# Performance work log

Hardware: AMD Instinct MI355X
Metric: run time of the kernel (lower is better)

## Reference

```python
import jax, jax.numpy as jnp
import numpy as np

SCALE = 0.08838834764831845  # 1/sqrt(128)


def setup_inputs() -> dict:
    key = jax.random.key(0)
    k1, k2, k3, k4 = jax.random.split(key, 4)
    B, Sq, H, D = 1, 2048, 32, 128
    Skv, K = 4096, 256
    return {
        "q": jax.random.normal(k1, (B, Sq, H, D), jnp.float32),
        "kv": jax.random.normal(k2, (B, Skv, 2, D), jnp.float32),  # stacked K,V (MQA)
        "attn_sink": jax.random.normal(k3, (H,), jnp.float32),
        "topk_idxs": jax.random.randint(k4, (B, Sq, K), 0, Skv),
    }


def reference(q, kv, attn_sink, topk_idxs):
    # q:        [B, Sq, H, D]
    # kv:       [B, Skv, 2, D]  (index 0 = keys, 1 = values; shared across heads)
    # topk_idxs:[B, Sq, K]      per-query selected KV positions
    # attn_sink:[H]             per-head sink logit added to the softmax denominator
    B = q.shape[0]
    # Gather selected KV per query: [B, Sq, K, 2, D]
    gathered = kv[jnp.arange(B)[:, None, None], topk_idxs]
    k = gathered[..., 0, :]  # [B, Sq, K, D]
    v = gathered[..., 1, :]  # [B, Sq, K, D]

    scores = jnp.einsum("bqhd,bqkd->bqhk", q, k) * SCALE  # [B, Sq, H, K]
    sink = attn_sink[None, None, :, None]                  # [1, 1, H, 1]

    # Numerically stable softmax over K selected tokens + sink logit.
    m = jnp.maximum(jnp.max(scores, axis=-1, keepdims=True), sink)
    e = jnp.exp(scores - m)
    denom = jnp.sum(e, axis=-1, keepdims=True) + jnp.exp(sink - m)
    probs = e / denom                                      # sink absorbs leftover mass

    out = jnp.einsum("bqhk,bqkd->bqhd", probs, v)          # [B, Sq, H, D]
    return out
```

## Files before the change

kernel.cpp:

```cpp
#include <hip/hip_runtime.h>
#include <hip/hip_bf16.h>

#define SQ 2048
#define NH 32
#define DH 128
#define NK 256
#define SCALE 0.08838834764831845f
#define LOG2E 1.4426950408889634f

typedef __attribute__((ext_vector_type(8))) __bf16 bf16x8;
typedef __attribute__((ext_vector_type(4))) float floatx4;

#define QS_STRIDE 136
#define KS_STRIDE 136
#define VB_STRIDE 72
#define PB_STRIDE 264

#define OFF_KV   16896
#define OFF_TOPK 35328
#define OFF_SINK 36352
#define OFF_RED  36480
#define OFF_RED2 36992
#define SMEM_SZ  37504

__device__ __forceinline__ unsigned pk_bf16(float a, float b) {
  union { __hip_bfloat162 h2; unsigned u; } c;
  c.h2 = __float22bfloat162_rn(make_float2(a, b));
  return c.u;
}

__device__ __forceinline__ float fast_exp2(float x) {
#if __has_builtin(__builtin_amdgcn_exp2f)
  return __builtin_amdgcn_exp2f(x);
#else
  return exp2f(x);
#endif
}

template <int CTRL>
__device__ __forceinline__ float dpp_rot(float x) {
  int i = __builtin_bit_cast(int, x);
  i = __builtin_amdgcn_mov_dpp(i, CTRL, 0xF, 0xF, true);
  return __builtin_bit_cast(float, i);
}
#define RED16_MAX(v) { v = fmaxf(v, dpp_rot<0x121>(v)); v = fmaxf(v, dpp_rot<0x122>(v)); \
                       v = fmaxf(v, dpp_rot<0x124>(v)); v = fmaxf(v, dpp_rot<0x128>(v)); }
#define RED16_SUM(v) { v += dpp_rot<0x121>(v); v += dpp_rot<0x122>(v); \
                       v += dpp_rot<0x124>(v); v += dpp_rot<0x128>(v); }

__global__ __launch_bounds__(256) void kv_to_bf16(const float* __restrict__ kv,
                                                  unsigned short* __restrict__ kvb) {
  int i = blockIdx.x * 256 + threadIdx.x;
  float4 f = ((const float4*)kv)[i];
  uint2 o = { pk_bf16(f.x, f.y), pk_bf16(f.z, f.w) };
  ((uint2*)kvb)[i] = o;
}

struct KR { uint4 v[4]; };
struct VR { uint4 a, b, c, d; };

__device__ __forceinline__ KR k_load(const unsigned short* __restrict__ kvb,
                                     const int* __restrict__ tks, int c, int tid) {
  int r = tid >> 2, seg = tid & 3;
  int idx = tks[c * 64 + r];
  const uint4* p = (const uint4*)(kvb + (size_t)idx * 256 + seg * 32);
  KR k;
#pragma unroll
  for (int i = 0; i < 4; i++) k.v[i] = p[i];
  return k;
}

__device__ __forceinline__ void k_write(unsigned short* kvbuf, const KR& k, int tid) {
  int r = tid >> 2, seg = tid & 3;
  uint4* d = (uint4*)&kvbuf[r * KS_STRIDE + seg * 32];
#pragma unroll
  for (int i = 0; i < 4; i++) d[i] = k.v[i];
}

__device__ __forceinline__ VR v_load(const unsigned short* __restrict__ kvb,
                                     const int* tks, int c, int tid) {
  int rg = tid & 15, dg = tid >> 4;
  int r0 = rg * 4, d0 = dg * 8;
  int4 i4 = *(const int4*)&tks[c * 64 + r0];
  VR v;
  v.a = *(const uint4*)(kvb + (size_t)i4.x * 256 + 128 + d0);
  v.b = *(const uint4*)(kvb + (size_t)i4.y * 256 + 128 + d0);
  v.c = *(const uint4*)(kvb + (size_t)i4.z * 256 + 128 + d0);
  v.d = *(const uint4*)(kvb + (size_t)i4.w * 256 + 128 + d0);
  return v;
}

__device__ __forceinline__ void v_write(unsigned short* kvbuf, const VR& v, int tid) {
  int rg = tid & 15, dg = tid >> 4;
  int r0 = rg * 4, d0 = dg * 8;
  const unsigned* pa = (const unsigned*)&v.a;
  const unsigned* pb = (const unsigned*)&v.b;
  const unsigned* pc = (const unsigned*)&v.c;
  const unsigned* pd = (const unsigned*)&v.d;
#pragma unroll
  for (int w = 0; w < 4; w++) {
    unsigned lo01 = __builtin_amdgcn_perm(pb[w], pa[w], 0x05040100u);
    unsigned lo23 = __builtin_amdgcn_perm(pd[w], pc[w], 0x05040100u);
    unsigned hi01 = __builtin_amdgcn_perm(pb[w], pa[w], 0x07060302u);
    unsigned hi23 = __builtin_amdgcn_perm(pd[w], pc[w], 0x07060302u);
    uint2 lo = { lo01, lo23 }, hi = { hi01, hi23 };
    *(uint2*)&kvbuf[(d0 + 2 * w) * VB_STRIDE + r0] = lo;
    *(uint2*)&kvbuf[(d0 + 2 * w + 1) * VB_STRIDE + r0] = hi;
  }
}

__device__ __forceinline__ void gemm1(const unsigned short* kvbuf,
                                      const bf16x8 af[2][4], int nrow, int quad,
                                      floatx4& a0, floatx4& a1) {
  a0 = (floatx4){0.f, 0.f, 0.f, 0.f};
  a1 = (floatx4){0.f, 0.f, 0.f, 0.f};
#pragma unroll
  for (int ks = 0; ks < 4; ks++) {
    bf16x8 b = *(const bf16x8*)&kvbuf[nrow * KS_STRIDE + ks * 32 + quad * 8];
    a0 = __builtin_amdgcn_mfma_f32_16x16x32_bf16(af[0][ks], b, a0, 0, 0, 0);
    a1 = __builtin_amdgcn_mfma_f32_16x16x32_bf16(af[1][ks], b, a1, 0, 0, 0);
  }
}

__device__ __forceinline__ void pv_chunk(const unsigned short* pbuf,
                                         const unsigned short* kvbuf, int c,
                                         int wave, int quad, int l16,
                                         floatx4 oacc[2][2]) {
#pragma unroll
  for (int ks = 0; ks < 2; ks++) {
    int kof = c * 64 + ks * 32 + quad * 8;
    bf16x8 a0 = *(const bf16x8*)&pbuf[l16 * PB_STRIDE + kof];
    bf16x8 a1 = *(const bf16x8*)&pbuf[(16 + l16) * PB_STRIDE + kof];
    int kl = ks * 32 + quad * 8;
    bf16x8 b0 = *(const bf16x8*)&kvbuf[(wave * 32 + l16) * VB_STRIDE + kl];
    bf16x8 b1 = *(const bf16x8*)&kvbuf[(wave * 32 + 16 + l16) * VB_STRIDE + kl];
    oacc[0][0] = __builtin_amdgcn_mfma_f32_16x16x32_bf16(a0, b0, oacc[0][0], 0, 0, 0);
    oacc[0][1] = __builtin_amdgcn_mfma_f32_16x16x32_bf16(a0, b1, oacc[0][1], 0, 0, 0);
    oacc[1][0] = __builtin_amdgcn_mfma_f32_16x16x32_bf16(a1, b0, oacc[1][0], 0, 0, 0);
    oacc[1][1] = __builtin_amdgcn_mfma_f32_16x16x32_bf16(a1, b1, oacc[1][1], 0, 0, 0);
  }
}

__global__ __launch_bounds__(256, 4) void sparse_attn_kernel(
    const float* __restrict__ q, const unsigned short* __restrict__ kvb,
    const float* __restrict__ sink, const int* __restrict__ topk,
    float* __restrict__ out) {
  __shared__ __align__(16) char smem[SMEM_SZ];
  unsigned short* qs    = (unsigned short*)smem;
  unsigned short* pbuf  = (unsigned short*)smem;
  unsigned short* kvbuf = (unsigned short*)(smem + OFF_KV);
  int*   topk_s = (int*)(smem + OFF_TOPK);
  float* sink_s = (float*)(smem + OFF_SINK);
  float* red    = (float*)(smem + OFF_RED);
  float* red2   = (float*)(smem + OFF_RED2);

  const int tid = threadIdx.x;
  const int s = blockIdx.x;
  const int wave = tid >> 6;
  const int lane = tid & 63;
  const int quad = lane >> 4;
  const int l16 = lane & 15;
  const int* tkg = topk + (size_t)s * NK;

  topk_s[tid] = tkg[tid];
  if (tid < 32) sink_s[tid] = sink[tid] * LOG2E;
  {
    int r = tid >> 2, seg = tid & 3;
    int idx = tkg[r];
    const uint4* p = (const uint4*)(kvb + (size_t)idx * 256 + seg * 32);
    uint4* d = (uint4*)&kvbuf[r * KS_STRIDE + seg * 32];
#pragma unroll
    for (int i = 0; i < 4; i++) d[i] = p[i];
  }
  {
    const float QSC = SCALE * LOG2E;
    const float* qp = q + (size_t)s * (NH * DH);
    int h = tid >> 3, d0 = (tid & 7) * 16;
    const float4* src = (const float4*)(qp + h * DH + d0);
    float4 f0 = src[0], f1 = src[1], f2 = src[2], f3 = src[3];
    uint4 o0 = { pk_bf16(f0.x * QSC, f0.y * QSC), pk_bf16(f0.z * QSC, f0.w * QSC),
                 pk_bf16(f1.x * QSC, f1.y * QSC), pk_bf16(f1.z * QSC, f1.w * QSC) };
    uint4 o1 = { pk_bf16(f2.x * QSC, f2.y * QSC), pk_bf16(f2.z * QSC, f2.w * QSC),
                 pk_bf16(f3.x * QSC, f3.y * QSC), pk_bf16(f3.z * QSC, f3.w * QSC) };
    *(uint4*)&qs[h * QS_STRIDE + d0] = o0;
    *(uint4*)&qs[h * QS_STRIDE + d0 + 8] = o1;
  }
  KR k1 = k_load(kvb, tkg, 1, tid);
  __syncthreads();

  bf16x8 afrag[2][4];
#pragma unroll
  for (int mt = 0; mt < 2; mt++)
#pragma unroll
    for (int ks = 0; ks < 4; ks++)
      afrag[mt][ks] =
          *(const bf16x8*)&qs[(mt * 16 + l16) * QS_STRIDE + ks * 32 + quad * 8];

  const int nrow = wave * 16 + l16;

  floatx4 sc[4][2];
  gemm1(kvbuf, afrag, nrow, quad, sc[0][0], sc[0][1]);
  __syncthreads();
  k_write(kvbuf, k1, tid);
  KR k2 = k_load(kvb, topk_s, 2, tid);
  __syncthreads();

  gemm1(kvbuf, afrag, nrow, quad, sc[1][0], sc[1][1]);
  __syncthreads();
  k_write(kvbuf, k2, tid);
  KR k3 = k_load(kvb, topk_s, 3, tid);
  __syncthreads();

  gemm1(kvbuf, afrag, nrow, quad, sc[2][0], sc[2][1]);
  __syncthreads();
  k_write(kvbuf, k3, tid);
  VR v0 = v_load(kvb, topk_s, 0, tid);
  __syncthreads();

  gemm1(kvbuf, afrag, nrow, quad, sc[3][0], sc[3][1]);
  __syncthreads();
  v_write(kvbuf, v0, tid);
  VR v1 = v_load(kvb, topk_s, 1, tid);

  float mh[2][4];
#pragma unroll
  for (int mt = 0; mt < 2; mt++)
#pragma unroll
    for (int r = 0; r < 4; r++) {
      float v = fmaxf(fmaxf(sc[0][mt][r], sc[1][mt][r]),
                      fmaxf(sc[2][mt][r], sc[3][mt][r]));
      RED16_MAX(v);
      mh[mt][r] = v;
    }
  if (l16 == 0) {
#pragma unroll
    for (int mt = 0; mt < 2; mt++)
#pragma unroll
      for (int r = 0; r < 4; r++)
        red[wave * 32 + mt * 16 + quad * 4 + r] = mh[mt][r];
  }
  __syncthreads();
#pragma unroll
  for (int mt = 0; mt < 2; mt++)
#pragma unroll
    for (int r = 0; r < 4; r++) {
      int h = mt * 16 + quad * 4 + r;
      float v = sink_s[h];
#pragma unroll
      for (int w = 0; w < 4; w++) v = fmaxf(v, red[w * 32 + h]);
      mh[mt][r] = v;
    }
  float ps[2][4];
#pragma unroll
  for (int mt = 0; mt < 2; mt++)
#pragma unroll
    for (int r = 0; r < 4; r++) {
      float acc = 0.f;
#pragma unroll
      for (int c = 0; c < 4; c++) {
        float e = fast_exp2(sc[c][mt][r] - mh[mt][r]);
        sc[c][mt][r] = e;
        acc += e;
      }
      RED16_SUM(acc);
      ps[mt][r] = acc;
    }
  if (l16 == 0) {
#pragma unroll
    for (int mt = 0; mt < 2; mt++)
#pragma unroll
      for (int r = 0; r < 4; r++)
        red2[wave * 32 + mt * 16 + quad * 4 + r] = ps[mt][r];
  }
  __syncthreads();
  float inv[2][4];
#pragma unroll
  for (int mt = 0; mt < 2; mt++)
#pragma unroll
    for (int r = 0; r < 4; r++) {
      int h = mt * 16 + quad * 4 + r;
      float dd = fast_exp2(sink_s[h] - mh[mt][r]);
#pragma unroll
      for (int w = 0; w < 4; w++) dd += red2[w * 32 + h];
      inv[mt][r] = 1.0f / dd;
    }
#pragma unroll
  for (int c = 0; c < 4; c++)
#pragma unroll
    for (int mt = 0; mt < 2; mt++) {
      int col = c * 64 + wave * 16 + l16;
      unsigned short* pb = &pbuf[(mt * 16 + quad * 4) * PB_STRIDE + col];
      unsigned p01 = pk_bf16(sc[c][mt][0], sc[c][mt][1]);
      unsigned p23 = pk_bf16(sc[c][mt][2], sc[c][mt][3]);
      pb[0] = (unsigned short)p01;
      pb[PB_STRIDE] = (unsigned short)(p01 >> 16);
      pb[2 * PB_STRIDE] = (unsigned short)p23;
      pb[3 * PB_STRIDE] = (unsigned short)(p23 >> 16);
    }
  __syncthreads();

  floatx4 oacc[2][2];
#pragma unroll
  for (int mt = 0; mt < 2; mt++)
#pragma unroll
    for (int nt = 0; nt < 2; nt++)
      oacc[mt][nt] = (floatx4){0.f, 0.f, 0.f, 0.f};

  pv_chunk(pbuf, kvbuf, 0, wave, quad, l16, oacc);
  __syncthreads();
  v_write(kvbuf, v1, tid);
  VR v2 = v_load(kvb, topk_s, 2, tid);
  __syncthreads();

  pv_chunk(pbuf, kvbuf, 1, wave, quad, l16, oacc);
  __syncthreads();
  v_write(kvbuf, v2, tid);
  VR v3 = v_load(kvb, topk_s, 3, tid);
  __syncthreads();

  pv_chunk(pbuf, kvbuf, 2, wave, quad, l16, oacc);
  __syncthreads();
  v_write(kvbuf, v3, tid);
  __syncthreads();

  pv_chunk(pbuf, kvbuf, 3, wave, quad, l16, oacc);

  {
    float* op = out + (size_t)s * (NH * DH);
#pragma unroll
    for (int mt = 0; mt < 2; mt++)
#pragma unroll
      for (int nt = 0; nt < 2; nt++)
#pragma unroll
        for (int r4 = 0; r4 < 4; r4++) {
          int h = mt * 16 + quad * 4 + r4;
          int d = wave * 32 + nt * 16 + l16;
          op[h * DH + d] = oacc[mt][nt][r4] * inv[mt][r4];
        }
  }
}

extern "C" void kernel_launch(void* const* d_in, const int* in_sizes, int n_in,
                              void* d_out, int out_size, void* d_ws, size_t ws_size,
                              hipStream_t stream) {
  (void)in_sizes; (void)n_in; (void)out_size; (void)ws_size;
  const float* q    = (const float*)d_in[0];
  const float* kv   = (const float*)d_in[1];
  const float* sink = (const float*)d_in[2];
  const int*   topk = (const int*)d_in[3];
  float* out = (float*)d_out;
  unsigned short* kvb = (unsigned short*)d_ws;

  kv_to_bf16<<<dim3(1024), dim3(256), 0, stream>>>(kv, kvb);
  sparse_attn_kernel<<<dim3(SQ), dim3(256), 0, stream>>>(q, kvb, sink, topk, out);
}
```

Measured before the change: 113.9 us.

## Load K and Q fragments directly from global memory, skipping LDS staging

The QK^T stage now reads each K row's MFMA B-fragment straight from the bf16 KV buffer in global memory, using per-lane top-k indices, instead of staging K chunks through shared memory with barriers. Q is also converted to bf16 directly into registers, and sink values and top-k indices are read from global memory rather than shared copies. This removes many __syncthreads and LDS round trips in the score phase. The cost is uncoalesced 16-byte gathers per lane that rely on L2/L1 hits, plus the V staging now overlaps the score GEMMs. Since vbuf does not alias pbuf, writing V chunk 0 during the score phase appears safe.

```diff
diff --git a/kernel.cpp b/kernel.cpp
--- a/kernel.cpp
+++ b/kernel.cpp
@@ -11,17 +11,13 @@
 typedef __attribute__((ext_vector_type(8))) __bf16 bf16x8;
 typedef __attribute__((ext_vector_type(4))) float floatx4;
 
-#define QS_STRIDE 136
-#define KS_STRIDE 136
 #define VB_STRIDE 72
 #define PB_STRIDE 264
 
-#define OFF_KV   16896
-#define OFF_TOPK 35328
-#define OFF_SINK 36352
-#define OFF_RED  36480
-#define OFF_RED2 36992
-#define SMEM_SZ  37504
+#define OFF_VB   16896
+#define OFF_RED  35328
+#define OFF_RED2 35840
+#define SMEM_SZ  36352
 
 __device__ __forceinline__ unsigned pk_bf16(float a, float b) {
   union { __hip_bfloat162 h2; unsigned u; } c;
@@ -56,32 +52,13 @@
   ((uint2*)kvb)[i] = o;
 }
 
-struct KR { uint4 v[4]; };
 struct VR { uint4 a, b, c, d; };
 
-__device__ __forceinline__ KR k_load(const unsigned short* __restrict__ kvb,
-                                     const int* __restrict__ tks, int c, int tid) {
-  int r = tid >> 2, seg = tid & 3;
-  int idx = tks[c * 64 + r];
-  const uint4* p = (const uint4*)(kvb + (size_t)idx * 256 + seg * 32);
-  KR k;
-#pragma unroll
-  for (int i = 0; i < 4; i++) k.v[i] = p[i];
-  return k;
-}
-
-__device__ __forceinline__ void k_write(unsigned short* kvbuf, const KR& k, int tid) {
-  int r = tid >> 2, seg = tid & 3;
-  uint4* d = (uint4*)&kvbuf[r * KS_STRIDE + seg * 32];
-#pragma unroll
-  for (int i = 0; i < 4; i++) d[i] = k.v[i];
-}
-
 __device__ __forceinline__ VR v_load(const unsigned short* __restrict__ kvb,
-                                     const int* tks, int c, int tid) {
+                                     const int* __restrict__ tkg, int c, int tid) {
   int rg = tid & 15, dg = tid >> 4;
   int r0 = rg * 4, d0 = dg * 8;
-  int4 i4 = *(const int4*)&tks[c * 64 + r0];
+  int4 i4 = *(const int4*)&tkg[c * 64 + r0];
   VR v;
   v.a = *(const uint4*)(kvb + (size_t)i4.x * 256 + 128 + d0);
   v.b = *(const uint4*)(kvb + (size_t)i4.y * 256 + 128 + d0);
@@ -90,7 +67,7 @@
   return v;
 }
 
-__device__ __forceinline__ void v_write(unsigned short* kvbuf, const VR& v, int tid) {
+__device__ __forceinline__ void v_write(unsigned short* vbuf, const VR& v, int tid) {
   int rg = tid & 15, dg = tid >> 4;
   int r0 = rg * 4, d0 = dg * 8;
   const unsigned* pa = (const unsigned*)&v.a;
@@ -104,26 +81,27 @@
     unsigned hi01 = __builtin_amdgcn_perm(pb[w], pa[w], 0x07060302u);
     unsigned hi23 = __builtin_amdgcn_perm(pd[w], pc[w], 0x07060302u);
     uint2 lo = { lo01, lo23 }, hi = { hi01, hi23 };
-    *(uint2*)&kvbuf[(d0 + 2 * w) * VB_STRIDE + r0] = lo;
-    *(uint2*)&kvbuf[(d0 + 2 * w + 1) * VB_STRIDE + r0] = hi;
-  }
-}
-
-__device__ __forceinline__ void gemm1(const unsigned short* kvbuf,
-                                      const bf16x8 af[2][4], int nrow, int quad,
-                                      floatx4& a0, floatx4& a1) {
+    *(uint2*)&vbuf[(d0 + 2 * w) * VB_STRIDE + r0] = lo;
+    *(uint2*)&vbuf[(d0 + 2 * w + 1) * VB_STRIDE + r0] = hi;
+  }
+}
+
+__device__ __forceinline__ void gemm1_direct(const unsigned short* __restrict__ kvb,
+                                             int idx, const bf16x8 af[2][4], int quad,
+                                             floatx4& a0, floatx4& a1) {
+  const unsigned short* kp = kvb + (size_t)idx * 256 + quad * 8;
   a0 = (floatx4){0.f, 0.f, 0.f, 0.f};
   a1 = (floatx4){0.f, 0.f, 0.f, 0.f};
 #pragma unroll
   for (int ks = 0; ks < 4; ks++) {
-    bf16x8 b = *(const bf16x8*)&kvbuf[nrow * KS_STRIDE + ks * 32 + quad * 8];
+    bf16x8 b = *(const bf16x8*)(kp + ks * 32);
     a0 = __builtin_amdgcn_mfma_f32_16x16x32_bf16(af[0][ks], b, a0, 0, 0, 0);
     a1 = __builtin_amdgcn_mfma_f32_16x16x32_bf16(af[1][ks], b, a1, 0, 0, 0);
   }
 }
 
 __device__ __forceinline__ void pv_chunk(const unsigned short* pbuf,
-                                         const unsigned short* kvbuf, int c,
+                                         const unsigned short* vbuf, int c,
                                          int wave, int quad, int l16,
                                          floatx4 oacc[2][2]) {
 #pragma unroll
@@ -132,8 +110,8 @@
     bf16x8 a0 = *(const bf16x8*)&pbuf[l16 * PB_STRIDE + kof];
     bf16x8 a1 = *(const bf16x8*)&pbuf[(16 + l16) * PB_STRIDE + kof];
     int kl = ks * 32 + quad * 8;
-    bf16x8 b0 = *(const bf16x8*)&kvbuf[(wave * 32 + l16) * VB_STRIDE + kl];
-    bf16x8 b1 = *(const bf16x8*)&kvbuf[(wave * 32 + 16 + l16) * VB_STRIDE + kl];
+    bf16x8 b0 = *(const bf16x8*)&vbuf[(wave * 32 + l16) * VB_STRIDE + kl];
+    bf16x8 b1 = *(const bf16x8*)&vbuf[(wave * 32 + 16 + l16) * VB_STRIDE + kl];
     oacc[0][0] = __builtin_amdgcn_mfma_f32_16x16x32_bf16(a0, b0, oacc[0][0], 0, 0, 0);
     oacc[0][1] = __builtin_amdgcn_mfma_f32_16x16x32_bf16(a0, b1, oacc[0][1], 0, 0, 0);
     oacc[1][0] = __builtin_amdgcn_mfma_f32_16x16x32_bf16(a1, b0, oacc[1][0], 0, 0, 0);
@@ -146,13 +124,10 @@
     const float* __restrict__ sink, const int* __restrict__ topk,
     float* __restrict__ out) {
   __shared__ __align__(16) char smem[SMEM_SZ];
-  unsigned short* qs    = (unsigned short*)smem;
-  unsigned short* pbuf  = (unsigned short*)smem;
-  unsigned short* kvbuf = (unsigned short*)(smem + OFF_KV);
-  int*   topk_s = (int*)(smem + OFF_TOPK);
-  float* sink_s = (float*)(smem + OFF_SINK);
-  float* red    = (float*)(smem + OFF_RED);
-  float* red2   = (float*)(smem + OFF_RED2);
+  unsigned short* pbuf = (unsigned short*)smem;
+  unsigned short* vbuf = (unsigned short*)(smem + OFF_VB);
+  float* red  = (float*)(smem + OFF_RED);
+  float* red2 = (float*)(smem + OFF_RED2);
 
   const int tid = threadIdx.x;
   const int s = blockIdx.x;
@@ -162,65 +137,40 @@
   const int l16 = lane & 15;
   const int* tkg = topk + (size_t)s * NK;
 
-  topk_s[tid] = tkg[tid];
-  if (tid < 32) sink_s[tid] = sink[tid] * LOG2E;
-  {
-    int r = tid >> 2, seg = tid & 3;
-    int idx = tkg[r];
-    const uint4* p = (const uint4*)(kvb + (size_t)idx * 256 + seg * 32);
-    uint4* d = (uint4*)&kvbuf[r * KS_STRIDE + seg * 32];
-#pragma unroll
-    for (int i = 0; i < 4; i++) d[i] = p[i];
-  }
-  {
-    const float QSC = SCALE * LOG2E;
-    const float* qp = q + (size_t)s * (NH * DH);
-    int h = tid >> 3, d0 = (tid & 7) * 16;
-    const float4* src = (const float4*)(qp + h * DH + d0);
-    float4 f0 = src[0], f1 = src[1], f2 = src[2], f3 = src[3];
-    uint4 o0 = { pk_bf16(f0.x * QSC, f0.y * QSC), pk_bf16(f0.z * QSC, f0.w * QSC),
-                 pk_bf16(f1.x * QSC, f1.y * QSC), pk_bf16(f1.z * QSC, f1.w * QSC) };
-    uint4 o1 = { pk_bf16(f2.x * QSC, f2.y * QSC), pk_bf16(f2.z * QSC, f2.w * QSC),
-                 pk_bf16(f3.x * QSC, f3.y * QSC), pk_bf16(f3.z * QSC, f3.w * QSC) };
-    *(uint4*)&qs[h * QS_STRIDE + d0] = o0;
-    *(uint4*)&qs[h * QS_STRIDE + d0 + 8] = o1;
-  }
-  KR k1 = k_load(kvb, tkg, 1, tid);
-  __syncthreads();
-
+  float snk[2][4];
+#pragma unroll
+  for (int mt = 0; mt < 2; mt++)
+#pragma unroll
+    for (int r = 0; r < 4; r++)
+      snk[mt][r] = sink[mt * 16 + quad * 4 + r] * LOG2E;
+
+  int kidx[4];
+#pragma unroll
+  for (int c = 0; c < 4; c++) kidx[c] = tkg[c * 64 + wave * 16 + l16];
+
+  const float QSC = SCALE * LOG2E;
+  const float* qp = q + (size_t)s * (NH * DH);
   bf16x8 afrag[2][4];
 #pragma unroll
   for (int mt = 0; mt < 2; mt++)
 #pragma unroll
-    for (int ks = 0; ks < 4; ks++)
-      afrag[mt][ks] =
-          *(const bf16x8*)&qs[(mt * 16 + l16) * QS_STRIDE + ks * 32 + quad * 8];
-
-  const int nrow = wave * 16 + l16;
+    for (int ks = 0; ks < 4; ks++) {
+      const float* base = qp + (mt * 16 + l16) * DH + ks * 32 + quad * 8;
+      float4 f0 = ((const float4*)base)[0];
+      float4 f1 = ((const float4*)base)[1];
+      uint4 u = { pk_bf16(f0.x * QSC, f0.y * QSC), pk_bf16(f0.z * QSC, f0.w * QSC),
+                  pk_bf16(f1.x * QSC, f1.y * QSC), pk_bf16(f1.z * QSC, f1.w * QSC) };
+      afrag[mt][ks] = __builtin_bit_cast(bf16x8, u);
+    }
 
   floatx4 sc[4][2];
-  gemm1(kvbuf, afrag, nrow, quad, sc[0][0], sc[0][1]);
-  __syncthreads();
-  k_write(kvbuf, k1, tid);
-  KR k2 = k_load(kvb, topk_s, 2, tid);
-  __syncthreads();
-
-  gemm1(kvbuf, afrag, nrow, quad, sc[1][0], sc[1][1]);
-  __syncthreads();
-  k_write(kvbuf, k2, tid);
-  KR k3 = k_load(kvb, topk_s, 3, tid);
-  __syncthreads();
-
-  gemm1(kvbuf, afrag, nrow, quad, sc[2][0], sc[2][1]);
-  __syncthreads();
-  k_write(kvbuf, k3, tid);
-  VR v0 = v_load(kvb, topk_s, 0, tid);
-  __syncthreads();
-
-  gemm1(kvbuf, afrag, nrow, quad, sc[3][0], sc[3][1]);
-  __syncthreads();
-  v_write(kvbuf, v0, tid);
-  VR v1 = v_load(kvb, topk_s, 1, tid);
+  gemm1_direct(kvb, kidx[0], afrag, quad, sc[0][0], sc[0][1]);
+  VR v0 = v_load(kvb, tkg, 0, tid);
+  gemm1_direct(kvb, kidx[1], afrag, quad, sc[1][0], sc[1][1]);
+  v_write(vbuf, v0, tid);
+  gemm1_direct(kvb, kidx[2], afrag, quad, sc[2][0], sc[2][1]);
+  VR v1 = v_load(kvb, tkg, 1, tid);
+  gemm1_direct(kvb, kidx[3], afrag, quad, sc[3][0], sc[3][1]);
 
   float mh[2][4];
 #pragma unroll
@@ -245,7 +195,7 @@
 #pragma unroll
     for (int r = 0; r < 4; r++) {
       int h = mt * 16 + quad * 4 + r;
-      float v = sink_s[h];
+      float v = snk[mt][r];
 #pragma unroll
       for (int w = 0; w < 4; w++) v = fmaxf(v, red[w * 32 + h]);
       mh[mt][r] = v;
@@ -278,10 +228,9 @@
   for (int mt = 0; mt < 2; mt++)
 #pragma unroll
     for (int r = 0; r < 4; r++) {
-      int h = mt * 16 + quad * 4 + r;
-      float dd = fast_exp2(sink_s[h] - mh[mt][r]);
-#pragma unroll
-      for (int w = 0; w < 4; w++) dd += red2[w * 32 + h];
+      float dd = fast_exp2(snk[mt][r] - mh[mt][r]);
+#pragma unroll
+      for (int w = 0; w < 4; w++) dd += red2[w * 32 + mt * 16 + quad * 4 + r];
       inv[mt][r] = 1.0f / dd;
     }
 #pragma unroll
@@ -306,24 +255,24 @@
     for (int nt = 0; nt < 2; nt++)
       oacc[mt][nt] = (floatx4){0.f, 0.f, 0.f, 0.f};
 
-  pv_chunk(pbuf, kvbuf, 0, wave, quad, l16, oacc);
-  __syncthreads();
-  v_write(kvbuf, v1, tid);
-  VR v2 = v_load(kvb, topk_s, 2, tid);
-  __syncthreads();
-
-  pv_chunk(pbuf, kvbuf, 1, wave, quad, l16, oacc);
-  __syncthreads();
-  v_write(kvbuf, v2, tid);
-  VR v3 = v_load(kvb, topk_s, 3, tid);
-  __syncthreads();
-
-  pv_chunk(pbuf, kvbuf, 2, wave, quad, l16, oacc);
-  __syncthreads();
-  v_write(kvbuf, v3, tid);
-  __syncthreads();
-
-  pv_chunk(pbuf, kvbuf, 3, wave, quad, l16, oacc);
+  pv_chunk(pbuf, vbuf, 0, wave, quad, l16, oacc);
+  __syncthreads();
+  v_write(vbuf, v1, tid);
+  VR v2 = v_load(kvb, tkg, 2, tid);
+  __syncthreads();
+
+  pv_chunk(pbuf, vbuf, 1, wave, quad, l16, oacc);
+  __syncthreads();
+  v_write(vbuf, v2, tid);
+  VR v3 = v_load(kvb, tkg, 3, tid);
+  __syncthreads();
+
+  pv_chunk(pbuf, vbuf, 2, wave, quad, l16, oacc);
+  __syncthreads();
+  v_write(vbuf, v3, tid);
+  __syncthreads();
+
+  pv_chunk(pbuf, vbuf, 3, wave, quad, l16, oacc);
 
   {
     float* op = out + (size_t)s * (NH * DH);
```

Measured after the change: 129.4 us. +13.6%, slower.

## Deepen gather prefetch, load Q fragments directly to registers, raise MFMA priority

Applied to the files above, without the earlier changes.

Q is read straight from global memory into MFMA fragment registers, so the shared-memory staging of Q goes away. The topk and sink shared copies are removed as well, with indices read from global memory and sink values held in registers. K and V gathers are issued two chunks ahead instead of one, and sched_barrier pins keep those loads early to hide gather latency. s_setprio is raised around the MFMA loops. The deeper prefetch holds more registers live, which risks spilling or lower occupancy under the launch bound of 4 blocks.

```diff
diff --git a/kernel.cpp b/kernel.cpp
--- a/kernel.cpp
+++ b/kernel.cpp
@@ -11,17 +11,16 @@
 typedef __attribute__((ext_vector_type(8))) __bf16 bf16x8;
 typedef __attribute__((ext_vector_type(4))) float floatx4;
 
-#define QS_STRIDE 136
 #define KS_STRIDE 136
 #define VB_STRIDE 72
 #define PB_STRIDE 264
 
 #define OFF_KV   16896
-#define OFF_TOPK 35328
-#define OFF_SINK 36352
-#define OFF_RED  36480
-#define OFF_RED2 36992
-#define SMEM_SZ  37504
+#define OFF_RED  35328
+#define OFF_RED2 35840
+#define SMEM_SZ  36352
+
+#define SCHED_PIN() __builtin_amdgcn_sched_barrier(0)
 
 __device__ __forceinline__ unsigned pk_bf16(float a, float b) {
   union { __hip_bfloat162 h2; unsigned u; } c;
@@ -60,9 +59,9 @@
 struct VR { uint4 a, b, c, d; };
 
 __device__ __forceinline__ KR k_load(const unsigned short* __restrict__ kvb,
-                                     const int* __restrict__ tks, int c, int tid) {
+                                     const int* __restrict__ tkg, int c, int tid) {
   int r = tid >> 2, seg = tid & 3;
-  int idx = tks[c * 64 + r];
+  int idx = tkg[c * 64 + r];
   const uint4* p = (const uint4*)(kvb + (size_t)idx * 256 + seg * 32);
   KR k;
 #pragma unroll
@@ -78,10 +77,10 @@
 }
 
 __device__ __forceinline__ VR v_load(const unsigned short* __restrict__ kvb,
-                                     const int* tks, int c, int tid) {
+                                     const int* __restrict__ tkg, int c, int tid) {
   int rg = tid & 15, dg = tid >> 4;
   int r0 = rg * 4, d0 = dg * 8;
-  int4 i4 = *(const int4*)&tks[c * 64 + r0];
+  int4 i4 = *(const int4*)&tkg[c * 64 + r0];
   VR v;
   v.a = *(const uint4*)(kvb + (size_t)i4.x * 256 + 128 + d0);
   v.b = *(const uint4*)(kvb + (size_t)i4.y * 256 + 128 + d0);
@@ -114,18 +113,21 @@
                                       floatx4& a0, floatx4& a1) {
   a0 = (floatx4){0.f, 0.f, 0.f, 0.f};
   a1 = (floatx4){0.f, 0.f, 0.f, 0.f};
+  __builtin_amdgcn_s_setprio(1);
 #pragma unroll
   for (int ks = 0; ks < 4; ks++) {
     bf16x8 b = *(const bf16x8*)&kvbuf[nrow * KS_STRIDE + ks * 32 + quad * 8];
     a0 = __builtin_amdgcn_mfma_f32_16x16x32_bf16(af[0][ks], b, a0, 0, 0, 0);
     a1 = __builtin_amdgcn_mfma_f32_16x16x32_bf16(af[1][ks], b, a1, 0, 0, 0);
   }
+  __builtin_amdgcn_s_setprio(0);
 }
 
 __device__ __forceinline__ void pv_chunk(const unsigned short* pbuf,
                                          const unsigned short* kvbuf, int c,
                                          int wave, int quad, int l16,
                                          floatx4 oacc[2][2]) {
+  __builtin_amdgcn_s_setprio(1);
 #pragma unroll
   for (int ks = 0; ks < 2; ks++) {
     int kof = c * 64 + ks * 32 + quad * 8;
@@ -139,6 +141,7 @@
     oacc[1][0] = __builtin_amdgcn_mfma_f32_16x16x32_bf16(a1, b0, oacc[1][0], 0, 0, 0);
     oacc[1][1] = __builtin_amdgcn_mfma_f32_16x16x32_bf16(a1, b1, oacc[1][1], 0, 0, 0);
   }
+  __builtin_amdgcn_s_setprio(0);
 }
 
 __global__ __launch_bounds__(256, 4) void sparse_attn_kernel(
@@ -146,13 +149,10 @@
     const float* __restrict__ sink, const int* __restrict__ topk,
     float* __restrict__ out) {
   __shared__ __align__(16) char smem[SMEM_SZ];
-  unsigned short* qs    = (unsigned short*)smem;
   unsigned short* pbuf  = (unsigned short*)smem;
   unsigned short* kvbuf = (unsigned short*)(smem + OFF_KV);
-  int*   topk_s = (int*)(smem + OFF_TOPK);
-  float* sink_s = (float*)(smem + OFF_SINK);
-  float* red    = (float*)(smem + OFF_RED);
-  float* red2   = (float*)(smem + OFF_RED2);
+  float* red  = (float*)(smem + OFF_RED);
+  float* red2 = (float*)(smem + OFF_RED2);
 
   const int tid = threadIdx.x;
   const int s = blockIdx.x;
@@ -162,39 +162,43 @@
   const int l16 = lane & 15;
   const int* tkg = topk + (size_t)s * NK;
 
-  topk_s[tid] = tkg[tid];
-  if (tid < 32) sink_s[tid] = sink[tid] * LOG2E;
-  {
-    int r = tid >> 2, seg = tid & 3;
-    int idx = tkg[r];
-    const uint4* p = (const uint4*)(kvb + (size_t)idx * 256 + seg * 32);
-    uint4* d = (uint4*)&kvbuf[r * KS_STRIDE + seg * 32];
-#pragma unroll
-    for (int i = 0; i < 4; i++) d[i] = p[i];
-  }
-  {
-    const float QSC = SCALE * LOG2E;
-    const float* qp = q + (size_t)s * (NH * DH);
-    int h = tid >> 3, d0 = (tid & 7) * 16;
-    const float4* src = (const float4*)(qp + h * DH + d0);
-    float4 f0 = src[0], f1 = src[1], f2 = src[2], f3 = src[3];
-    uint4 o0 = { pk_bf16(f0.x * QSC, f0.y * QSC), pk_bf16(f0.z * QSC, f0.w * QSC),
-                 pk_bf16(f1.x * QSC, f1.y * QSC), pk_bf16(f1.z * QSC, f1.w * QSC) };
-    uint4 o1 = { pk_bf16(f2.x * QSC, f2.y * QSC), pk_bf16(f2.z * QSC, f2.w * QSC),
-                 pk_bf16(f3.x * QSC, f3.y * QSC), pk_bf16(f3.z * QSC, f3.w * QSC) };
-    *(uint4*)&qs[h * QS_STRIDE + d0] = o0;
-    *(uint4*)&qs[h * QS_STRIDE + d0 + 8] = o1;
-  }
+  KR k0 = k_load(kvb, tkg, 0, tid);
+  SCHED_PIN();
+
+  const float QSC = SCALE * LOG2E;
+  const float* qp = q + (size_t)s * (NH * DH);
+  float4 qf[2][4][2];
+#pragma unroll
+  for (int mt = 0; mt < 2; mt++)
+#pragma unroll
+    for (int ks = 0; ks < 4; ks++) {
+      const float* base = qp + (mt * 16 + l16) * DH + ks * 32 + quad * 8;
+      qf[mt][ks][0] = ((const float4*)base)[0];
+      qf[mt][ks][1] = ((const float4*)base)[1];
+    }
   KR k1 = k_load(kvb, tkg, 1, tid);
-  __syncthreads();
+  KR k2 = k_load(kvb, tkg, 2, tid);
+  SCHED_PIN();
+
+  float snk[2][4];
+#pragma unroll
+  for (int mt = 0; mt < 2; mt++)
+#pragma unroll
+    for (int r = 0; r < 4; r++)
+      snk[mt][r] = sink[mt * 16 + quad * 4 + r] * LOG2E;
 
   bf16x8 afrag[2][4];
 #pragma unroll
   for (int mt = 0; mt < 2; mt++)
 #pragma unroll
-    for (int ks = 0; ks < 4; ks++)
-      afrag[mt][ks] =
-          *(const bf16x8*)&qs[(mt * 16 + l16) * QS_STRIDE + ks * 32 + quad * 8];
+    for (int ks = 0; ks < 4; ks++) {
+      float4 f0 = qf[mt][ks][0], f1 = qf[mt][ks][1];
+      uint4 u = { pk_bf16(f0.x * QSC, f0.y * QSC), pk_bf16(f0.z * QSC, f0.w * QSC),
+                  pk_bf16(f1.x * QSC, f1.y * QSC), pk_bf16(f1.z * QSC, f1.w * QSC) };
+      afrag[mt][ks] = __builtin_bit_cast(bf16x8, u);
+    }
+  k_write(kvbuf, k0, tid);
+  __syncthreads();
 
   const int nrow = wave * 16 + l16;
 
@@ -202,25 +206,27 @@
   gemm1(kvbuf, afrag, nrow, quad, sc[0][0], sc[0][1]);
   __syncthreads();
   k_write(kvbuf, k1, tid);
-  KR k2 = k_load(kvb, topk_s, 2, tid);
+  KR k3 = k_load(kvb, tkg, 3, tid);
+  SCHED_PIN();
   __syncthreads();
 
   gemm1(kvbuf, afrag, nrow, quad, sc[1][0], sc[1][1]);
   __syncthreads();
   k_write(kvbuf, k2, tid);
-  KR k3 = k_load(kvb, topk_s, 3, tid);
+  VR v0 = v_load(kvb, tkg, 0, tid);
+  SCHED_PIN();
   __syncthreads();
 
   gemm1(kvbuf, afrag, nrow, quad, sc[2][0], sc[2][1]);
   __syncthreads();
   k_write(kvbuf, k3, tid);
-  VR v0 = v_load(kvb, topk_s, 0, tid);
+  VR v1 = v_load(kvb, tkg, 1, tid);
+  SCHED_PIN();
   __syncthreads();
 
   gemm1(kvbuf, afrag, nrow, quad, sc[3][0], sc[3][1]);
   __syncthreads();
   v_write(kvbuf, v0, tid);
-  VR v1 = v_load(kvb, topk_s, 1, tid);
 
   float mh[2][4];
 #pragma unroll
@@ -240,12 +246,14 @@
         red[wave * 32 + mt * 16 + quad * 4 + r] = mh[mt][r];
   }
   __syncthreads();
+  VR v2 = v_load(kvb, tkg, 2, tid);
+  SCHED_PIN();
 #pragma unroll
   for (int mt = 0; mt < 2; mt++)
 #pragma unroll
     for (int r = 0; r < 4; r++) {
       int h = mt * 16 + quad * 4 + r;
-      float v = sink_s[h];
+      float v = snk[mt][r];
 #pragma unroll
       for (int w = 0; w < 4; w++) v = fmaxf(v, red[w * 32 + h]);
       mh[mt][r] = v;
@@ -278,10 +286,9 @@
   for (int mt = 0; mt < 2; mt++)
 #pragma unroll
     for (int r = 0; r < 4; r++) {
-      int h = mt * 16 + quad * 4 + r;
-      float dd = fast_exp2(sink_s[h] - mh[mt][r]);
-#pragma unroll
-      for (int w = 0; w < 4; w++) dd += red2[w * 32 + h];
+      float dd = fast_exp2(snk[mt][r] - mh[mt][r]);
+#pragma unroll
+      for (int w = 0; w < 4; w++) dd += red2[w * 32 + mt * 16 + quad * 4 + r];
       inv[mt][r] = 1.0f / dd;
     }
 #pragma unroll
@@ -306,16 +313,16 @@
     for (int nt = 0; nt < 2; nt++)
       oacc[mt][nt] = (floatx4){0.f, 0.f, 0.f, 0.f};
 
+  VR v3 = v_load(kvb, tkg, 3, tid);
+  SCHED_PIN();
   pv_chunk(pbuf, kvbuf, 0, wave, quad, l16, oacc);
   __syncthreads();
   v_write(kvbuf, v1, tid);
-  VR v2 = v_load(kvb, topk_s, 2, tid);
   __syncthreads();
 
   pv_chunk(pbuf, kvbuf, 1, wave, quad, l16, oacc);
   __syncthreads();
   v_write(kvbuf, v2, tid);
-  VR v3 = v_load(kvb, topk_s, 3, tid);
   __syncthreads();
 
   pv_chunk(pbuf, kvbuf, 2, wave, quad, l16, oacc);
```

After: 129.1 us. +13.3%, slower.
